# Kernel tuning notes

Hardware: AMD Instinct MI355X
Metric: run time of the kernel (lower is better)

## Reference

```python
import jax, jax.numpy as jnp
import numpy as np

B, S, D_MODEL, H = 2, 2048, 1024, 16
D = D_MODEL // H  # 64 per-head dim


def setup_inputs() -> dict:
    key = jax.random.key(0)
    ks = jax.random.split(key, 9)
    scale = 1.0 / np.sqrt(D_MODEL)
    x = jax.random.normal(ks[0], (B, S, D_MODEL), dtype=jnp.float32)
    # per-head Q/K/V linears stacked: [H, d_model, d] weights, [H, d] biases
    Wq = jax.random.uniform(ks[1], (H, D_MODEL, D), jnp.float32, -scale, scale)
    bq = jax.random.uniform(ks[2], (H, D), jnp.float32, -scale, scale)
    Wk = jax.random.uniform(ks[3], (H, D_MODEL, D), jnp.float32, -scale, scale)
    bk = jax.random.uniform(ks[4], (H, D), jnp.float32, -scale, scale)
    Wv = jax.random.uniform(ks[5], (H, D_MODEL, D), jnp.float32, -scale, scale)
    bv = jax.random.uniform(ks[6], (H, D), jnp.float32, -scale, scale)
    # output projection: [d_model, d_model] weight, [d_model] bias
    Wo = jax.random.uniform(ks[7], (D_MODEL, D_MODEL), jnp.float32, -scale, scale)
    bo = jax.random.uniform(ks[8], (D_MODEL,), jnp.float32, -scale, scale)
    return {"x": x, "Wq": Wq, "bq": bq, "Wk": Wk, "bk": bk,
            "Wv": Wv, "bv": bv, "Wo": Wo, "bo": bo}


def reference(x, Wq, bq, Wk, bk, Wv, bv, Wo, bo):
    # batched per-head projections (equivalent to H separate nn.Linear's)
    Q = jnp.einsum('bsm,hmd->bhsd', x, Wq) + bq[None, :, None, :]
    K = jnp.einsum('bsm,hmd->bhsd', x, Wk) + bk[None, :, None, :]
    V = jnp.einsum('bsm,hmd->bhsd', x, Wv) + bv[None, :, None, :]
    scores = jnp.einsum('bhsd,bhtd->bhst', Q, K) / jnp.sqrt(jnp.float32(D))
    attn = jax.nn.softmax(scores, axis=-1)  # [B,H,S,S]
    out = jnp.einsum('bhst,bhtd->bhsd', attn, V)
    # concat heads along feature dim: [B,S,H*D]
    out = out.transpose(0, 2, 1, 3).reshape(B, S, D_MODEL)
    # output projection; dropout is identity in eval mode
    return out @ Wo + bo
```

## Files before the change

kernel.cpp:

```cpp
#include <hip/hip_runtime.h>
#include <hip/hip_bf16.h>

#define DEV __device__ __forceinline__

typedef unsigned short u16;
typedef __attribute__((ext_vector_type(8))) short bf16x8;
typedef __attribute__((ext_vector_type(4))) float f32x4;
typedef __attribute__((ext_vector_type(16))) float f32x16;
typedef __attribute__((ext_vector_type(4))) unsigned short us4;
typedef __attribute__((ext_vector_type(2))) unsigned u32x2;

DEV void gld_lds16(const void* g, void* l) {
  __builtin_amdgcn_global_load_lds((const __attribute__((address_space(1))) void*)g,
                                   (__attribute__((address_space(3))) void*)l, 16, 0, 0);
}

DEV u16 f2bf(float x) {
  union { float f; unsigned u; } v; v.f = x;
  unsigned r = v.u + 0x7FFFu + ((v.u >> 16) & 1u);
  return (u16)(r >> 16);
}

DEV float ex2(float x) {
  float r; asm("v_exp_f32 %0, %1" : "=v"(r) : "v"(x)); return r;
}

DEV unsigned cvtpk(float a, float b) {
  unsigned r; asm("v_cvt_pk_bf16_f32 %0, %1, %2" : "=v"(r) : "v"(a), "v"(b)); return r;
}

__global__ __launch_bounds__(256) void k_cast_x(const float* __restrict__ x, u16* __restrict__ xb) {
  int i = (blockIdx.x * 256 + threadIdx.x) * 4;
  const float4 v = *(const float4*)(x + i);
  us4 o; o.x = f2bf(v.x); o.y = f2bf(v.y); o.z = f2bf(v.z); o.w = f2bf(v.w);
  *(us4*)(xb + i) = o;
}

__global__ __launch_bounds__(256) void k_prep_w(const float* __restrict__ Wq, const float* __restrict__ Wk,
                                                const float* __restrict__ Wv, const float* __restrict__ Wo,
                                                u16* __restrict__ wqkt, u16* __restrict__ wvt,
                                                u16* __restrict__ wot) {
  __shared__ float t[64][65];
  const int bb = blockIdx.x, tid = threadIdx.x;
  const float* src; u16* dst; int src_ld, dst_row0, dst_col0;
  if (bb < 768) {
    int which = bb >> 8, h = (bb >> 4) & 15, m0 = (bb & 15) * 64;
    const float* W = which == 0 ? Wq : (which == 1 ? Wk : Wv);
    src = W + h * 65536 + m0 * 64; src_ld = 64;
    dst = (which == 2) ? wvt : (wqkt + (which == 1 ? (1024 * 1024) : 0));
    dst_row0 = h * 64; dst_col0 = m0;
  } else {
    int t2 = bb - 768, mt = t2 >> 4, nt = t2 & 15;
    src = Wo + (size_t)(mt * 64) * 1024 + nt * 64; src_ld = 1024;
    dst = wot; dst_row0 = nt * 64; dst_col0 = mt * 64;
  }
  {
    int r = tid >> 2, c0 = (tid & 3) * 16;
    const float* s = src + (size_t)r * src_ld + c0;
#pragma unroll
    for (int q = 0; q < 4; ++q) {
      float4 v = *(const float4*)(s + q * 4);
      t[r][c0 + q * 4 + 0] = v.x; t[r][c0 + q * 4 + 1] = v.y;
      t[r][c0 + q * 4 + 2] = v.z; t[r][c0 + q * 4 + 3] = v.w;
    }
  }
  __syncthreads();
  {
    int d = tid >> 2, mb = (tid & 3) * 16;
    bf16x8 v0, v1;
#pragma unroll
    for (int e = 0; e < 8; ++e) {
      v0[e] = (short)f2bf(t[mb + e][d]);
      v1[e] = (short)f2bf(t[mb + 8 + e][d]);
    }
    u16* dp = dst + (size_t)(dst_row0 + d) * 1024 + dst_col0 + mb;
    *(bf16x8*)(dp) = v0;
    *(bf16x8*)(dp + 8) = v1;
  }
}

template <int MODE>
__global__ __launch_bounds__(256) void k_gemm(const u16* __restrict__ A, const u16* __restrict__ Bt,
                                              const float* __restrict__ b0, const float* __restrict__ b1,
                                              u16* __restrict__ outb, float* __restrict__ outf) {
  constexpr int K = 1024;
  __shared__ __align__(16) u16 As[128 * 64];
  __shared__ __align__(16) u16 Bs[128 * 64];
  const int tid = threadIdx.x, wid = tid >> 6, lane = tid & 63;
  const int lo = lane & 15, hi = lane >> 4;
  const int wr = wid >> 1, wc = wid & 1;
  const int bm = blockIdx.y, bn = blockIdx.x;
  const u16* Ab = A + (size_t)bm * 128 * K;
  const u16* Bb = Bt + (size_t)bn * 128 * K;
  const int sr = lane >> 3, sc = lane & 7;
  f32x4 acc[4][4] = {};
  for (int k0 = 0; k0 < K; k0 += 64) {
    __syncthreads();
#pragma unroll
    for (int i = 0; i < 4; ++i) {
      int r = wid * 32 + i * 8 + sr;
      int cs = sc ^ (r & 7);
      gld_lds16(Ab + (size_t)r * K + k0 + cs * 8, As + (wid * 32 + i * 8) * 64);
      gld_lds16(Bb + (size_t)r * K + k0 + cs * 8, Bs + (wid * 32 + i * 8) * 64);
    }
    __syncthreads();
#pragma unroll
    for (int ks = 0; ks < 2; ++ks) {
      bf16x8 af[4], bfr[4];
#pragma unroll
      for (int mt = 0; mt < 4; ++mt) {
        int r = wr * 64 + mt * 16 + lo;
        int c = (hi + 4 * ks) ^ (r & 7);
        af[mt] = *(const bf16x8*)(As + r * 64 + c * 8);
      }
#pragma unroll
      for (int nt = 0; nt < 4; ++nt) {
        int r = wc * 64 + nt * 16 + lo;
        int c = (hi + 4 * ks) ^ (r & 7);
        bfr[nt] = *(const bf16x8*)(Bs + r * 64 + c * 8);
      }
#pragma unroll
      for (int mt = 0; mt < 4; ++mt)
#pragma unroll
        for (int nt = 0; nt < 4; ++nt)
          acc[mt][nt] = __builtin_amdgcn_mfma_f32_16x16x32_bf16(af[mt], bfr[nt], acc[mt][nt], 0, 0, 0);
    }
  }
#pragma unroll
  for (int mt = 0; mt < 4; ++mt) {
#pragma unroll
    for (int nt = 0; nt < 4; ++nt) {
      const int i0 = bm * 128 + wr * 64 + mt * 16 + hi * 4;
      const int j = bn * 128 + wc * 64 + nt * 16 + lo;
#pragma unroll
      for (int rg = 0; rg < 4; ++rg) {
        const int i = i0 + rg;
        float v = acc[mt][nt][rg];
        if (MODE == 0) {
          v += (j < 1024) ? b0[j] : b1[j - 1024];
          if (j < 1024) v *= 0.18033688011112042f;
          outb[(size_t)i * 2048 + j] = f2bf(v);
        } else if (MODE == 1) {
          v += b0[i];
          outb[(size_t)((j >> 11) * 1024 + i) * 2048 + (j & 2047)] = f2bf(v);
        } else {
          v += b0[j];
          outf[(size_t)i * 1024 + j] = v;
        }
      }
    }
  }
}

__global__ __launch_bounds__(256, 2) void k_attn(const u16* __restrict__ qk, const u16* __restrict__ vt,
                                                 u16* __restrict__ ao) {
  __shared__ __align__(16) u16 Kl[2][64 * 64];
  __shared__ __align__(16) u16 Vl[2][64 * 64];
  const int tid = threadIdx.x, wid = tid >> 6, lane = tid & 63;
  const int ql = lane & 31, Lh = lane >> 5;
  const int qb = blockIdx.x & 15, bh = blockIdx.x >> 4;
  const int b = bh >> 4, h = bh & 15;
  const int qg = qb * 128 + wid * 32 + ql;

  bf16x8 qB[4];
  const u16* qrow = qk + (size_t)(b * 2048 + qg) * 2048 + h * 64;
#pragma unroll
  for (int kd = 0; kd < 4; ++kd) qB[kd] = *(const bf16x8*)(qrow + kd * 16 + Lh * 8);

  const u16* Kg = qk + 1024 + (size_t)b * 2048 * 2048 + h * 64;
  const u16* Vg = vt + (size_t)bh * 64 * 2048;
  const int sr = lane >> 3, sc = lane & 7;

  f32x16 acco[2] = {};
  float m_run = -1e30f, l_part = 0.f;

#pragma unroll
  for (int i = 0; i < 2; ++i) {
    int r = wid * 16 + i * 8 + sr;
    int cs = sc ^ (r & 7);
    gld_lds16(Kg + (size_t)r * 2048 + cs * 8, Kl[0] + (wid * 16 + i * 8) * 64);
    gld_lds16(Vg + (size_t)r * 2048 + cs * 8, Vl[0] + (wid * 16 + i * 8) * 64);
  }

  for (int it = 0; it < 32; ++it) {
    __syncthreads();
    if (it + 1 < 32) {
      const int t0 = (it + 1) * 64, bufn = (it + 1) & 1;
#pragma unroll
      for (int i = 0; i < 2; ++i) {
        int r = wid * 16 + i * 8 + sr;
        int cs = sc ^ (r & 7);
        gld_lds16(Kg + (size_t)(t0 + r) * 2048 + cs * 8, Kl[bufn] + (wid * 16 + i * 8) * 64);
        gld_lds16(Vg + (size_t)r * 2048 + t0 + cs * 8, Vl[bufn] + (wid * 16 + i * 8) * 64);
      }
    }
    const u16* Kb = Kl[it & 1];
    const u16* Vb = Vl[it & 1];

    f32x16 accs[2] = {};
#pragma unroll
    for (int kd = 0; kd < 4; ++kd) {
      int cg = 2 * kd + Lh;
#pragma unroll
      for (int tt = 0; tt < 2; ++tt) {
        int r = tt * 32 + ql;
        bf16x8 ka = *(const bf16x8*)(Kb + r * 64 + (cg ^ (r & 7)) * 8);
        accs[tt] = __builtin_amdgcn_mfma_f32_32x32x16_bf16(ka, qB[kd], accs[tt], 0, 0, 0);
      }
    }

    bf16x8 vf[2][4];
#pragma unroll
    for (int dt = 0; dt < 2; ++dt)
#pragma unroll
      for (int kt = 0; kt < 4; ++kt) {
        int r = dt * 32 + ql;
        int cg = 2 * kt + Lh;
        vf[dt][kt] = *(const bf16x8*)(Vb + r * 64 + (cg ^ (r & 7)) * 8);
      }

    float t8[8];
#pragma unroll
    for (int m = 0; m < 8; ++m)
      t8[m] = fmaxf(fmaxf(accs[0][2 * m], accs[0][2 * m + 1]),
                    fmaxf(accs[1][2 * m], accs[1][2 * m + 1]));
    float mx = fmaxf(fmaxf(fmaxf(t8[0], t8[1]), fmaxf(t8[2], t8[3])),
                     fmaxf(fmaxf(t8[4], t8[5]), fmaxf(t8[6], t8[7])));

    if (__any(mx > m_run + 8.f)) {
      float mxw = fmaxf(mx, __shfl_xor(mx, 32));
      float mnew = fmaxf(m_run, mxw);
      float al = ex2(m_run - mnew);
      m_run = mnew;
      l_part *= al;
      acco[0] *= al;
      acco[1] *= al;
    }

    unsigned dw[2][8];
    float ls0 = 0.f, ls1 = 0.f;
#pragma unroll
    for (int tt = 0; tt < 2; ++tt)
#pragma unroll
      for (int m = 0; m < 8; ++m) {
        float p0 = ex2(accs[tt][2 * m] - m_run);
        float p1 = ex2(accs[tt][2 * m + 1] - m_run);
        if (m & 1) ls1 += p0 + p1; else ls0 += p0 + p1;
        dw[tt][m] = cvtpk(p0, p1);
      }
    l_part += ls0 + ls1;

#pragma unroll
    for (int kt = 0; kt < 4; ++kt) {
      const int tt = kt >> 1, c = kt & 1;
      u32x2 s0 = __builtin_amdgcn_permlane32_swap(dw[tt][4 * c + 0], dw[tt][4 * c + 2], false, false);
      u32x2 s1 = __builtin_amdgcn_permlane32_swap(dw[tt][4 * c + 1], dw[tt][4 * c + 3], false, false);
      union { unsigned u[4]; bf16x8 v; } pb;
      pb.u[0] = s0[0]; pb.u[1] = s1[0]; pb.u[2] = s0[1]; pb.u[3] = s1[1];
#pragma unroll
      for (int dt = 0; dt < 2; ++dt)
        acco[dt] = __builtin_amdgcn_mfma_f32_32x32x16_bf16(vf[dt][kt], pb.v, acco[dt], 0, 0, 0);
    }
  }

  float lsum = l_part + __shfl_xor(l_part, 32);
  float inv = 1.f / lsum;
  u16* orow = ao + (size_t)(b * 2048 + qg) * 1024 + h * 64;
#pragma unroll
  for (int dt = 0; dt < 2; ++dt)
#pragma unroll
    for (int g = 0; g < 4; ++g) {
      float o0 = acco[dt][4 * g + 0] * inv, o1 = acco[dt][4 * g + 1] * inv;
      float o2 = acco[dt][4 * g + 2] * inv, o3 = acco[dt][4 * g + 3] * inv;
      uint2 w; w.x = cvtpk(o0, o1); w.y = cvtpk(o2, o3);
      *(uint2*)(orow + dt * 32 + g * 8 + Lh * 4) = w;
    }
}

extern "C" void kernel_launch(void* const* d_in, const int* in_sizes, int n_in,
                              void* d_out, int out_size, void* d_ws, size_t ws_size,
                              hipStream_t stream) {
  const float* x  = (const float*)d_in[0];
  const float* Wq = (const float*)d_in[1];
  const float* bq = (const float*)d_in[2];
  const float* Wk = (const float*)d_in[3];
  const float* bk = (const float*)d_in[4];
  const float* Wv = (const float*)d_in[5];
  const float* bv = (const float*)d_in[6];
  const float* Wo = (const float*)d_in[7];
  const float* bo = (const float*)d_in[8];
  float* out = (float*)d_out;

  char* ws = (char*)d_ws;
  u16* xb   = (u16*)(ws);
  u16* wqkt = (u16*)(ws + (8u << 20));
  u16* wvt  = (u16*)(ws + (12u << 20));
  u16* wot  = (u16*)(ws + (14u << 20));
  u16* qk   = (u16*)(ws + (16u << 20));
  u16* vt   = (u16*)(ws + (32u << 20));
  u16* aob  = (u16*)(ws + (40u << 20));

  k_cast_x<<<4096, 256, 0, stream>>>(x, xb);
  k_prep_w<<<1024, 256, 0, stream>>>(Wq, Wk, Wv, Wo, wqkt, wvt, wot);
  k_gemm<0><<<dim3(16, 32), 256, 0, stream>>>(xb, wqkt, bq, bk, qk, nullptr);
  k_gemm<1><<<dim3(32, 8), 256, 0, stream>>>(wvt, xb, bv, nullptr, vt, nullptr);
  k_attn<<<512, 256, 0, stream>>>(qk, vt, aob);
  k_gemm<2><<<dim3(8, 32), 256, 0, stream>>>(aob, wot, bo, nullptr, nullptr, out);
}
```

Measured before the change: 135.5 us.

## Split attention KV range across two wave groups and merge partial softmax in LDS

The attention kernel now launches 512 threads per block, with two groups of four waves each processing half of the key/value sequence for the same 128 queries. At the end, the partial outputs and softmax statistics are merged through shared memory. The block index is also remapped so neighbouring blocks spread across batch and heads. This doubles the waves in flight per query tile to hide latency and shortens each wave's serial loop, at the cost of more LDS, an extra merge phase with two barriers, and higher register pressure under the new launch bounds.

```diff
diff --git a/kernel.cpp b/kernel.cpp
--- a/kernel.cpp
+++ b/kernel.cpp
@@ -152,23 +152,27 @@
   }
 }
 
-__global__ __launch_bounds__(256, 2) void k_attn(const u16* __restrict__ qk, const u16* __restrict__ vt,
+__global__ __launch_bounds__(512, 4) void k_attn(const u16* __restrict__ qk, const u16* __restrict__ vt,
                                                  u16* __restrict__ ao) {
-  __shared__ __align__(16) u16 Kl[2][64 * 64];
-  __shared__ __align__(16) u16 Vl[2][64 * 64];
+  __shared__ __align__(16) u16 smem[32768];
   const int tid = threadIdx.x, wid = tid >> 6, lane = tid & 63;
   const int ql = lane & 31, Lh = lane >> 5;
-  const int qb = blockIdx.x & 15, bh = blockIdx.x >> 4;
+  const int tg = wid >> 2, qw = wid & 3;
+  const int logical = (blockIdx.x & 7) * 64 + (blockIdx.x >> 3);
+  const int qb = logical & 15, bh = logical >> 4;
   const int b = bh >> 4, h = bh & 15;
-  const int qg = qb * 128 + wid * 32 + ql;
+  const int qg = qb * 128 + qw * 32 + ql;
+
+  u16* const Kbase = smem + tg * 2 * 4096;
+  u16* const Vbase = smem + 16384 + tg * 2 * 4096;
 
   bf16x8 qB[4];
   const u16* qrow = qk + (size_t)(b * 2048 + qg) * 2048 + h * 64;
 #pragma unroll
   for (int kd = 0; kd < 4; ++kd) qB[kd] = *(const bf16x8*)(qrow + kd * 16 + Lh * 8);
 
-  const u16* Kg = qk + 1024 + (size_t)b * 2048 * 2048 + h * 64;
-  const u16* Vg = vt + (size_t)bh * 64 * 2048;
+  const u16* Kg = qk + 1024 + (size_t)b * 2048 * 2048 + (size_t)tg * 1024 * 2048 + h * 64;
+  const u16* Vg = vt + (size_t)bh * 64 * 2048 + tg * 1024;
   const int sr = lane >> 3, sc = lane & 7;
 
   f32x16 acco[2] = {};
@@ -176,26 +180,26 @@
 
 #pragma unroll
   for (int i = 0; i < 2; ++i) {
-    int r = wid * 16 + i * 8 + sr;
+    int r = qw * 16 + i * 8 + sr;
     int cs = sc ^ (r & 7);
-    gld_lds16(Kg + (size_t)r * 2048 + cs * 8, Kl[0] + (wid * 16 + i * 8) * 64);
-    gld_lds16(Vg + (size_t)r * 2048 + cs * 8, Vl[0] + (wid * 16 + i * 8) * 64);
-  }
-
-  for (int it = 0; it < 32; ++it) {
+    gld_lds16(Kg + (size_t)r * 2048 + cs * 8, Kbase + (qw * 16 + i * 8) * 64);
+    gld_lds16(Vg + (size_t)r * 2048 + cs * 8, Vbase + (qw * 16 + i * 8) * 64);
+  }
+
+  for (int it = 0; it < 16; ++it) {
     __syncthreads();
-    if (it + 1 < 32) {
-      const int t0 = (it + 1) * 64, bufn = (it + 1) & 1;
+    if (it + 1 < 16) {
+      const int t0 = (it + 1) * 64, bo2 = ((it + 1) & 1) * 4096;
 #pragma unroll
       for (int i = 0; i < 2; ++i) {
-        int r = wid * 16 + i * 8 + sr;
+        int r = qw * 16 + i * 8 + sr;
         int cs = sc ^ (r & 7);
-        gld_lds16(Kg + (size_t)(t0 + r) * 2048 + cs * 8, Kl[bufn] + (wid * 16 + i * 8) * 64);
-        gld_lds16(Vg + (size_t)r * 2048 + t0 + cs * 8, Vl[bufn] + (wid * 16 + i * 8) * 64);
-      }
-    }
-    const u16* Kb = Kl[it & 1];
-    const u16* Vb = Vl[it & 1];
+        gld_lds16(Kg + (size_t)(t0 + r) * 2048 + cs * 8, Kbase + bo2 + (qw * 16 + i * 8) * 64);
+        gld_lds16(Vg + (size_t)r * 2048 + t0 + cs * 8, Vbase + bo2 + (qw * 16 + i * 8) * 64);
+      }
+    }
+    const u16* Kb = Kbase + (it & 1) * 4096;
+    const u16* Vb = Vbase + (it & 1) * 4096;
 
     f32x16 accs[2] = {};
 #pragma unroll
@@ -263,18 +267,43 @@
     }
   }
 
-  float lsum = l_part + __shfl_xor(l_part, 32);
-  float inv = 1.f / lsum;
-  u16* orow = ao + (size_t)(b * 2048 + qg) * 1024 + h * 64;
-#pragma unroll
-  for (int dt = 0; dt < 2; ++dt)
-#pragma unroll
-    for (int g = 0; g < 4; ++g) {
-      float o0 = acco[dt][4 * g + 0] * inv, o1 = acco[dt][4 * g + 1] * inv;
-      float o2 = acco[dt][4 * g + 2] * inv, o3 = acco[dt][4 * g + 3] * inv;
-      uint2 w; w.x = cvtpk(o0, o1); w.y = cvtpk(o2, o3);
-      *(uint2*)(orow + dt * 32 + g * 8 + Lh * 4) = w;
-    }
+  float lp = l_part + __shfl_xor(l_part, 32);
+  __syncthreads();
+  float* Om = (float*)smem;
+  float* Ml = (float*)(smem + 17408);
+  float* Ll = (float*)(smem + 17664);
+
+  if (tg == 1) {
+#pragma unroll
+    for (int dt = 0; dt < 2; ++dt)
+#pragma unroll
+      for (int g = 0; g < 4; ++g) {
+        f32x4 w = { acco[dt][4 * g + 0], acco[dt][4 * g + 1],
+                    acco[dt][4 * g + 2], acco[dt][4 * g + 3] };
+        *(f32x4*)(Om + (qw * 32 + ql) * 68 + dt * 32 + g * 8 + Lh * 4) = w;
+      }
+    if (Lh == 0) { Ml[qw * 32 + ql] = m_run; Ll[qw * 32 + ql] = lp; }
+  }
+  __syncthreads();
+  if (tg == 0) {
+    const float m1 = Ml[qw * 32 + ql], l1 = Ll[qw * 32 + ql];
+    const float ms = fmaxf(m_run, m1);
+    const float a0 = ex2(m_run - ms), a1 = ex2(m1 - ms);
+    const float inv = 1.f / (lp * a0 + l1 * a1);
+    u16* orow = ao + (size_t)(b * 2048 + qg) * 1024 + h * 64;
+#pragma unroll
+    for (int dt = 0; dt < 2; ++dt)
+#pragma unroll
+      for (int g = 0; g < 4; ++g) {
+        f32x4 o1 = *(const f32x4*)(Om + (qw * 32 + ql) * 68 + dt * 32 + g * 8 + Lh * 4);
+        float o0f = (acco[dt][4 * g + 0] * a0 + o1[0] * a1) * inv;
+        float o1f = (acco[dt][4 * g + 1] * a0 + o1[1] * a1) * inv;
+        float o2f = (acco[dt][4 * g + 2] * a0 + o1[2] * a1) * inv;
+        float o3f = (acco[dt][4 * g + 3] * a0 + o1[3] * a1) * inv;
+        uint2 w; w.x = cvtpk(o0f, o1f); w.y = cvtpk(o2f, o3f);
+        *(uint2*)(orow + dt * 32 + g * 8 + Lh * 4) = w;
+      }
+  }
 }
 
 extern "C" void kernel_launch(void* const* d_in, const int* in_sizes, int n_in,
@@ -304,6 +333,6 @@
   k_prep_w<<<1024, 256, 0, stream>>>(Wq, Wk, Wv, Wo, wqkt, wvt, wot);
   k_gemm<0><<<dim3(16, 32), 256, 0, stream>>>(xb, wqkt, bq, bk, qk, nullptr);
   k_gemm<1><<<dim3(32, 8), 256, 0, stream>>>(wvt, xb, bv, nullptr, vt, nullptr);
-  k_attn<<<512, 256, 0, stream>>>(qk, vt, aob);
+  k_attn<<<512, 512, 0, stream>>>(qk, vt, aob);
   k_gemm<2><<<dim3(8, 32), 256, 0, stream>>>(aob, wot, bo, nullptr, nullptr, out);
 }
```

Measured after the change: 152.1 us. 12.2% more time.

## Double-buffer GEMM LDS tiles and triple-buffer attention K/V prefetch

Applied to the files above, without the earlier changes.

The GEMM kernel now keeps two LDS buffers for the A and B tiles. It prefetches the next k-slice while running MFMAs on the current one, so each step needs one wait and one barrier instead of two syncthreads. The attention kernel moves to three K/V LDS buffers with prefetch distance two, using a partial vmcnt wait so a tile's loads can stay in flight across an iteration. It also raises the attention launch-bounds occupancy hint from 2 to 3. The costs are twice the LDS per GEMM block, which may lower occupancy, and a tighter attention register budget that could cause spills.

```diff
diff --git a/kernel.cpp b/kernel.cpp
--- a/kernel.cpp
+++ b/kernel.cpp
@@ -84,8 +84,8 @@
                                               const float* __restrict__ b0, const float* __restrict__ b1,
                                               u16* __restrict__ outb, float* __restrict__ outf) {
   constexpr int K = 1024;
-  __shared__ __align__(16) u16 As[128 * 64];
-  __shared__ __align__(16) u16 Bs[128 * 64];
+  __shared__ __align__(16) u16 As[2][128 * 64];
+  __shared__ __align__(16) u16 Bs[2][128 * 64];
   const int tid = threadIdx.x, wid = tid >> 6, lane = tid & 63;
   const int lo = lane & 15, hi = lane >> 4;
   const int wr = wid >> 1, wc = wid & 1;
@@ -94,16 +94,29 @@
   const u16* Bb = Bt + (size_t)bn * 128 * K;
   const int sr = lane >> 3, sc = lane & 7;
   f32x4 acc[4][4] = {};
-  for (int k0 = 0; k0 < K; k0 += 64) {
-    __syncthreads();
-#pragma unroll
-    for (int i = 0; i < 4; ++i) {
-      int r = wid * 32 + i * 8 + sr;
-      int cs = sc ^ (r & 7);
-      gld_lds16(Ab + (size_t)r * K + k0 + cs * 8, As + (wid * 32 + i * 8) * 64);
-      gld_lds16(Bb + (size_t)r * K + k0 + cs * 8, Bs + (wid * 32 + i * 8) * 64);
-    }
-    __syncthreads();
+
+#pragma unroll
+  for (int i = 0; i < 4; ++i) {
+    int r = wid * 32 + i * 8 + sr;
+    int cs = sc ^ (r & 7);
+    gld_lds16(Ab + (size_t)r * K + cs * 8, &As[0][(wid * 32 + i * 8) * 64]);
+    gld_lds16(Bb + (size_t)r * K + cs * 8, &Bs[0][(wid * 32 + i * 8) * 64]);
+  }
+
+  int cur = 0;
+  for (int kt = 0; kt < 16; ++kt) {
+    asm volatile("s_waitcnt vmcnt(0)" ::: "memory");
+    __builtin_amdgcn_s_barrier();
+    if (kt + 1 < 16) {
+      const int k0 = (kt + 1) * 64;
+#pragma unroll
+      for (int i = 0; i < 4; ++i) {
+        int r = wid * 32 + i * 8 + sr;
+        int cs = sc ^ (r & 7);
+        gld_lds16(Ab + (size_t)r * K + k0 + cs * 8, &As[cur ^ 1][(wid * 32 + i * 8) * 64]);
+        gld_lds16(Bb + (size_t)r * K + k0 + cs * 8, &Bs[cur ^ 1][(wid * 32 + i * 8) * 64]);
+      }
+    }
 #pragma unroll
     for (int ks = 0; ks < 2; ++ks) {
       bf16x8 af[4], bfr[4];
@@ -111,13 +124,13 @@
       for (int mt = 0; mt < 4; ++mt) {
         int r = wr * 64 + mt * 16 + lo;
         int c = (hi + 4 * ks) ^ (r & 7);
-        af[mt] = *(const bf16x8*)(As + r * 64 + c * 8);
+        af[mt] = *(const bf16x8*)(&As[cur][r * 64 + c * 8]);
       }
 #pragma unroll
       for (int nt = 0; nt < 4; ++nt) {
         int r = wc * 64 + nt * 16 + lo;
         int c = (hi + 4 * ks) ^ (r & 7);
-        bfr[nt] = *(const bf16x8*)(Bs + r * 64 + c * 8);
+        bfr[nt] = *(const bf16x8*)(&Bs[cur][r * 64 + c * 8]);
       }
 #pragma unroll
       for (int mt = 0; mt < 4; ++mt)
@@ -125,6 +138,7 @@
         for (int nt = 0; nt < 4; ++nt)
           acc[mt][nt] = __builtin_amdgcn_mfma_f32_16x16x32_bf16(af[mt], bfr[nt], acc[mt][nt], 0, 0, 0);
     }
+    cur ^= 1;
   }
 #pragma unroll
   for (int mt = 0; mt < 4; ++mt) {
@@ -152,10 +166,10 @@
   }
 }
 
-__global__ __launch_bounds__(256, 2) void k_attn(const u16* __restrict__ qk, const u16* __restrict__ vt,
+__global__ __launch_bounds__(256, 3) void k_attn(const u16* __restrict__ qk, const u16* __restrict__ vt,
                                                  u16* __restrict__ ao) {
-  __shared__ __align__(16) u16 Kl[2][64 * 64];
-  __shared__ __align__(16) u16 Vl[2][64 * 64];
+  __shared__ __align__(16) u16 Kl[3][64 * 64];
+  __shared__ __align__(16) u16 Vl[3][64 * 64];
   const int tid = threadIdx.x, wid = tid >> 6, lane = tid & 63;
   const int ql = lane & 31, Lh = lane >> 5;
   const int qb = blockIdx.x & 15, bh = blockIdx.x >> 4;
@@ -175,27 +189,33 @@
   float m_run = -1e30f, l_part = 0.f;
 
 #pragma unroll
-  for (int i = 0; i < 2; ++i) {
-    int r = wid * 16 + i * 8 + sr;
-    int cs = sc ^ (r & 7);
-    gld_lds16(Kg + (size_t)r * 2048 + cs * 8, Kl[0] + (wid * 16 + i * 8) * 64);
-    gld_lds16(Vg + (size_t)r * 2048 + cs * 8, Vl[0] + (wid * 16 + i * 8) * 64);
-  }
-
+  for (int t = 0; t < 2; ++t)
+#pragma unroll
+    for (int i = 0; i < 2; ++i) {
+      int r = wid * 16 + i * 8 + sr;
+      int cs = sc ^ (r & 7);
+      gld_lds16(Kg + (size_t)(t * 64 + r) * 2048 + cs * 8, &Kl[t][(wid * 16 + i * 8) * 64]);
+      gld_lds16(Vg + (size_t)r * 2048 + t * 64 + cs * 8, &Vl[t][(wid * 16 + i * 8) * 64]);
+    }
+
+  int cur = 0;
   for (int it = 0; it < 32; ++it) {
-    __syncthreads();
-    if (it + 1 < 32) {
-      const int t0 = (it + 1) * 64, bufn = (it + 1) & 1;
+    if (it < 31) asm volatile("s_waitcnt vmcnt(4)" ::: "memory");
+    else         asm volatile("s_waitcnt vmcnt(0)" ::: "memory");
+    __builtin_amdgcn_s_barrier();
+    if (it + 2 < 32) {
+      int sb = cur + 2; if (sb >= 3) sb -= 3;
+      const int t0 = (it + 2) * 64;
 #pragma unroll
       for (int i = 0; i < 2; ++i) {
         int r = wid * 16 + i * 8 + sr;
         int cs = sc ^ (r & 7);
-        gld_lds16(Kg + (size_t)(t0 + r) * 2048 + cs * 8, Kl[bufn] + (wid * 16 + i * 8) * 64);
-        gld_lds16(Vg + (size_t)r * 2048 + t0 + cs * 8, Vl[bufn] + (wid * 16 + i * 8) * 64);
-      }
-    }
-    const u16* Kb = Kl[it & 1];
-    const u16* Vb = Vl[it & 1];
+        gld_lds16(Kg + (size_t)(t0 + r) * 2048 + cs * 8, &Kl[sb][(wid * 16 + i * 8) * 64]);
+        gld_lds16(Vg + (size_t)r * 2048 + t0 + cs * 8, &Vl[sb][(wid * 16 + i * 8) * 64]);
+      }
+    }
+    const u16* Kb = Kl[cur];
+    const u16* Vb = Vl[cur];
 
     f32x16 accs[2] = {};
 #pragma unroll
@@ -204,7 +224,7 @@
 #pragma unroll
       for (int tt = 0; tt < 2; ++tt) {
         int r = tt * 32 + ql;
-        bf16x8 ka = *(const bf16x8*)(Kb + r * 64 + (cg ^ (r & 7)) * 8);
+        bf16x8 ka = *(const bf16x8*)(Kb + r * 64 + ((cg ^ (r & 7)) * 8));
         accs[tt] = __builtin_amdgcn_mfma_f32_32x32x16_bf16(ka, qB[kd], accs[tt], 0, 0, 0);
       }
     }
@@ -216,7 +236,7 @@
       for (int kt = 0; kt < 4; ++kt) {
         int r = dt * 32 + ql;
         int cg = 2 * kt + Lh;
-        vf[dt][kt] = *(const bf16x8*)(Vb + r * 64 + (cg ^ (r & 7)) * 8);
+        vf[dt][kt] = *(const bf16x8*)(Vb + r * 64 + ((cg ^ (r & 7)) * 8));
       }
 
     float t8[8];
@@ -261,6 +281,8 @@
       for (int dt = 0; dt < 2; ++dt)
         acco[dt] = __builtin_amdgcn_mfma_f32_32x32x16_bf16(vf[dt][kt], pb.v, acco[dt], 0, 0, 0);
     }
+
+    cur = (cur == 2) ? 0 : cur + 1;
   }
 
   float lsum = l_part + __shfl_xor(l_part, 32);
```

Result: no change. 135.1 us (-0.3%).
